# Kernel optimization log

Measured on AMD Instinct MI355X. Metric: run time of the kernel, lower is better.

## Reference

```python
import jax, jax.numpy as jnp
import numpy as np
from jax import lax

DN = ('NCHW', 'OIHW', 'NCHW')

def conv(x, w, b):
    y = lax.conv_general_dilated(x, w, (1, 1), 'VALID', dimension_numbers=DN)
    return y + b[None, :, None, None]

def maxpool2(x):
    return lax.reduce_window(x, -jnp.inf, lax.max, (1, 1, 2, 2), (1, 1, 2, 2), 'VALID')

def setup_inputs() -> dict:
    key = jax.random.key(0)
    ks = jax.random.split(key, 16)
    s = 0.05
    return {
        'x': jax.random.normal(ks[0], (8192, 1, 28, 28), jnp.float32),
        'kf_w1': jax.random.normal(ks[1], (8, 1, 7, 7), jnp.float32) * s,
        'kf_b1': jax.random.normal(ks[2], (8,), jnp.float32) * s,
        'kf_w2': jax.random.normal(ks[3], (10, 8, 5, 5), jnp.float32) * s,
        'kf_b2': jax.random.normal(ks[4], (10,), jnp.float32) * s,
        'kf_fc1_w': jax.random.normal(ks[5], (32, 90), jnp.float32) * s,
        'kf_fc1_b': jax.random.normal(ks[6], (32,), jnp.float32) * s,
        'kf_fc2_w': jax.random.normal(ks[7], (40, 32), jnp.float32) * s,
        'kf_fc2_b': jax.random.normal(ks[8], (40,), jnp.float32) * s,
        'conv2_w': jax.random.normal(ks[9], (20, 10, 5, 5), jnp.float32) * s,
        'conv2_b': jax.random.normal(ks[10], (20,), jnp.float32) * s,
        'fc1_w': jax.random.normal(ks[11], (50, 320), jnp.float32) * s,
        'fc1_b': jax.random.normal(ks[12], (50,), jnp.float32) * s,
        'fc2_w': jax.random.normal(ks[13], (10, 50), jnp.float32) * s,
        'fc2_b': jax.random.normal(ks[14], (10,), jnp.float32) * s,
    }

def _forward(x, kf_w1, kf_b1, kf_w2, kf_b2, kf_fc1_w, kf_fc1_b, kf_fc2_w, kf_fc2_b,
             conv2_w, conv2_b, fc1_w, fc1_b, fc2_w, fc2_b):
    n = x.shape[0]
    # KernelFinder: conv7 -> pool -> relu -> conv5 -> pool -> relu
    f = jax.nn.relu(maxpool2(conv(x, kf_w1, kf_b1)))        # [N,8,11,11]
    f = jax.nn.relu(maxpool2(conv(f, kf_w2, kf_b2)))        # [N,10,3,3]
    f = f.reshape(n, 90)
    h = jax.nn.relu(f @ kf_fc1_w.T + kf_fc1_b)
    kernels = (h @ kf_fc2_w.T + kf_fc2_b).reshape(n, 10, 1, 2, 2)
    # per-sample dynamic conv: each image gets its own [10,1,2,2] kernel
    def one(img, k):
        return lax.conv_general_dilated(img[None], k, (1, 1), 'VALID',
                                        dimension_numbers=DN)[0]
    y = jax.vmap(one)(x, kernels)                           # [N,10,27,27]
    y = jax.nn.relu(maxpool2(y))                            # [N,10,13,13]
    # dropout2d is identity in eval mode
    y = jax.nn.relu(maxpool2(conv(y, conv2_w, conv2_b)))    # [N,20,4,4]
    y = y.reshape(n, 320)
    y = jax.nn.relu(y @ fc1_w.T + fc1_b)
    # F.dropout identity in eval
    y = y @ fc2_w.T + fc2_b
    return jax.nn.log_softmax(y, axis=1)

def reference(x, kf_w1, kf_b1, kf_w2, kf_b2, kf_fc1_w, kf_fc1_b, kf_fc2_w, kf_fc2_b,
              conv2_w, conv2_b, fc1_w, fc1_b, fc2_w, fc2_b):
    return _forward(x, kf_w1, kf_b1, kf_w2, kf_b2, kf_fc1_w, kf_fc1_b, kf_fc2_w,
                    kf_fc2_b, conv2_w, conv2_b, fc1_w, fc1_b, fc2_w, fc2_b)
```

## Files before the change

### kernel.cpp

```cpp
#include <hip/hip_runtime.h>
#include <math.h>

#define TPB 192

typedef __attribute__((ext_vector_type(8))) short bf16x8;
typedef __attribute__((ext_vector_type(4))) float f32x4;

#define OX    0
#define OC1   784
#define OY2   784
#define OF    2656
#define OH    2748
#define OC2S  2656
#define OK2   4960
#define OP3   0
#define OPF   320
#define OA1   420
#define OZ    472
#define SM_TOT 5000

#define W3_ENTRIES 15360

__device__ __forceinline__ unsigned short f2bf(float f) {
    unsigned int u = __float_as_uint(f);
    u += 0x7FFF + ((u >> 16) & 1);
    return (unsigned short)(u >> 16);
}

__global__ void repack_w3(const float* __restrict__ conv2_w,
                          unsigned short* __restrict__ w3)
{
    int i = blockIdx.x * blockDim.x + threadIdx.x;
    if (i >= W3_ENTRIES) return;
    int k  = i & 31;
    int oc = (i >> 5) & 31;
    int g  = i >> 10;
    int kyp = g % 3, kx = g / 3;
    int kyip = k >> 4, ic = k & 15, ky = 2 * kyp + kyip;
    float v = 0.f;
    if (oc < 20 && ic < 10 && ky < 5)
        v = conv2_w[(oc * 10 + ic) * 25 + ky * 5 + kx];
    w3[i] = f2bf(v);
}

__global__ __launch_bounds__(TPB) void fused_forward(
    const float* __restrict__ x,
    const float* __restrict__ kf_w1, const float* __restrict__ kf_b1,
    const float* __restrict__ kf_w2, const float* __restrict__ kf_b2,
    const float* __restrict__ kf_fc1_w, const float* __restrict__ kf_fc1_b,
    const float* __restrict__ kf_fc2_w, const float* __restrict__ kf_fc2_b,
    const float* __restrict__ conv2_w, const float* __restrict__ conv2_b,
    const float* __restrict__ fc1_w, const float* __restrict__ fc1_b,
    const float* __restrict__ fc2_w, const float* __restrict__ fc2_b,
    const unsigned short* __restrict__ w3,
    float* __restrict__ out)
{
    __shared__ __align__(16) float sm[SM_TOT];
    const int tid = threadIdx.x;
    const int n = blockIdx.x;

    {
        const float4* xg = (const float4*)(x + (long long)n * 784);
        float4* d = (float4*)&sm[OX];
        for (int i = tid; i < 196; i += TPB) d[i] = xg[i];
    }
    __syncthreads();

    if (tid < 176) {
        int oc = tid & 7;
        int r  = tid >> 3;
        int py = r >> 1;
        int h  = r & 1;
        const int cc0 = 10 * h;
        float c[2][12];
        #pragma unroll
        for (int r2 = 0; r2 < 2; ++r2)
            #pragma unroll
            for (int i = 0; i < 12; ++i) c[r2][i] = 0.f;
        float wc[7], wp[7];
        const float* wg = kf_w1 + oc * 49;
        #pragma unroll
        for (int i = 0; i < 7; ++i) wc[i] = wg[i];
        #pragma unroll
        for (int t = 0; t < 8; ++t) {
            const float2* xs = (const float2*)&sm[OX + (2 * py + t) * 28 + cc0];
            float row[18];
            #pragma unroll
            for (int i = 0; i < 9; ++i) { float2 q = xs[i]; row[2*i] = q.x; row[2*i+1] = q.y; }
            if (t <= 6) {
                #pragma unroll
                for (int kx = 0; kx < 7; ++kx)
                    #pragma unroll
                    for (int cc = 0; cc < 12; ++cc)
                        c[0][cc] = fmaf(wc[kx], row[cc + kx], c[0][cc]);
            }
            if (t >= 1) {
                #pragma unroll
                for (int kx = 0; kx < 7; ++kx)
                    #pragma unroll
                    for (int cc = 0; cc < 12; ++cc)
                        c[1][cc] = fmaf(wp[kx], row[cc + kx], c[1][cc]);
            }
            #pragma unroll
            for (int i = 0; i < 7; ++i) wp[i] = wc[i];
            if (t < 7) {
                const float* wn = wg + (t + 1) * 7;
                #pragma unroll
                for (int i = 0; i < 7; ++i) wc[i] = wn[i];
            }
        }
        float b = kf_b1[oc];
        #pragma unroll
        for (int j = 0; j < 6; ++j) {
            float m = fmaxf(fmaxf(c[0][2 * j], c[0][2 * j + 1]),
                            fmaxf(c[1][2 * j], c[1][2 * j + 1]));
            sm[OC1 + oc * 132 + py * 12 + 5 * h + j] = fmaxf(m + b, 0.f);
        }
    }
    __syncthreads();

    if (tid < 90) {
        int oc = tid % 10, r = tid / 10;
        int py = r / 3, px = r % 3;
        float a00 = 0.f, a01 = 0.f, a10 = 0.f, a11 = 0.f;
        for (int ic = 0; ic < 8; ++ic) {
            float w[25];
            const float* wg = kf_w2 + (oc * 8 + ic) * 25;
            #pragma unroll
            for (int i = 0; i < 25; ++i) w[i] = wg[i];
            const float* xb = &sm[OC1 + ic * 132 + 2 * py * 12 + 2 * px];
            float cur[6], nxt[6];
            {
                const float2* xr = (const float2*)xb;
                #pragma unroll
                for (int i = 0; i < 3; ++i) { float2 q = xr[i]; cur[2*i] = q.x; cur[2*i+1] = q.y; }
            }
            #pragma unroll
            for (int ky = 0; ky < 5; ++ky) {
                const float2* xr = (const float2*)(xb + (ky + 1) * 12);
                #pragma unroll
                for (int i = 0; i < 3; ++i) { float2 q = xr[i]; nxt[2*i] = q.x; nxt[2*i+1] = q.y; }
                #pragma unroll
                for (int kx = 0; kx < 5; ++kx) {
                    float wv = w[ky * 5 + kx];
                    a00 = fmaf(wv, cur[kx],     a00);
                    a01 = fmaf(wv, cur[kx + 1], a01);
                    a10 = fmaf(wv, nxt[kx],     a10);
                    a11 = fmaf(wv, nxt[kx + 1], a11);
                }
                #pragma unroll
                for (int i = 0; i < 6; ++i) cur[i] = nxt[i];
            }
        }
        float m = fmaxf(fmaxf(a00, a01), fmaxf(a10, a11)) + kf_b2[oc];
        sm[OF + oc * 9 + py * 3 + px] = fmaxf(m, 0.f);
    }
    __syncthreads();

    if (tid < 32) {
        float acc = kf_fc1_b[tid];
        const float2* wr = (const float2*)&kf_fc1_w[tid * 90];
        const float2* ff = (const float2*)&sm[OF];
        for (int i = 0; i < 45; ++i) {
            float2 wv = wr[i], fv = ff[i];
            acc = fmaf(wv.x, fv.x, acc);
            acc = fmaf(wv.y, fv.y, acc);
        }
        sm[OH + tid] = fmaxf(acc, 0.f);
    }
    if (tid < 40) {
        float acc = kf_fc2_b[tid];
        const float4* wr = (const float4*)&kf_fc2_w[tid * 32];
        const float4* hh = (const float4*)&sm[OH];
        #pragma unroll
        for (int i = 0; i < 8; ++i) {
            float4 wv = wr[i], hv = hh[i];
            acc = fmaf(wv.x, hv.x, acc);
            acc = fmaf(wv.y, hv.y, acc);
            acc = fmaf(wv.z, hv.z, acc);
            acc = fmaf(wv.w, hv.w, acc);
        }
        sm[OK2 + tid] = acc;
    }
    if (tid >= 64) {
        float4* z4 = (float4*)&sm[OY2];
        for (int i = tid - 64; i < 468; i += 128) z4[i] = float4{0.f, 0.f, 0.f, 0.f};
    }
    __syncthreads();

    if (tid < 120) {
        int oc = tid % 10, py = tid / 10;
        float4 kv = *(const float4*)&sm[OK2 + oc * 4];
        float k0 = kv.x, k1 = kv.y, k2 = kv.z, k3 = kv.w;
        const float* x0 = &sm[OX + 2 * py * 28];
        const float* x1 = x0 + 28;
        const float* x2 = x0 + 56;
        float2 q0 = *(const float2*)&x0[0];
        float2 q1 = *(const float2*)&x1[0];
        float2 q2 = *(const float2*)&x2[0];
        float A0 = q0.x, B0 = q0.y;
        float A1 = q1.x, B1 = q1.y;
        float A2 = q2.x, B2 = q2.y;
        unsigned short* y2 = (unsigned short*)&sm[OY2];
        #pragma unroll
        for (int j = 0; j < 12; ++j) {
            float2 r0 = *(const float2*)&x0[2 * j + 2];
            float2 r1 = *(const float2*)&x1[2 * j + 2];
            float2 r2v = *(const float2*)&x2[2 * j + 2];
            float C0 = r0.x, C1 = r1.x, C2 = r2v.x;
            float c00 = A0 * k0 + B0 * k1 + A1 * k2 + B1 * k3;
            float c01 = B0 * k0 + C0 * k1 + B1 * k2 + C1 * k3;
            float c10 = A1 * k0 + B1 * k1 + A2 * k2 + B2 * k3;
            float c11 = B1 * k0 + C1 * k1 + B2 * k2 + C2 * k3;
            float m = fmaxf(fmaxf(c00, c01), fmaxf(c10, c11));
            y2[py * 288 + j * 24 + oc] = f2bf(fmaxf(m, 0.f));
            A0 = C0; A1 = C1; A2 = C2;
            B0 = r0.y; B1 = r1.y; B2 = r2v.y;
        }
    }
    __syncthreads();

    {
        const int wv = tid >> 6;
        if (wv < 2) {
            const int l  = tid & 63;
            const int lm = l & 15, lk = l >> 4;
            f32x4 a00 = {0.f, 0.f, 0.f, 0.f};
            f32x4 a01 = a00, a10 = a00, a11 = a00;
            const char* W3 = (const char*)w3;
            const int aoff = (lm * 32 + lk * 8) * 2;
            const int n0 = wv * 32 + lm;
            const int n1 = n0 + 16;
            const int kyip = l >> 5, icb = (lk & 1) * 8;
            const unsigned short* Y2 = (const unsigned short*)&sm[OY2];
            const int b0 = ((n0 >> 3) + kyip) * 288 + (n0 & 7) * 24 + icb;
            const int b1 = ((n1 >> 3) + kyip) * 288 + (n1 & 7) * 24 + icb;
            #pragma unroll
            for (int p = 0; p < 3; ++p) {
                #pragma unroll
                for (int kx = 0; kx < 5; ++kx) {
                    const char* wa = W3 + (kx * 3 + p) * 2048 + aoff;
                    bf16x8 A0 = *(const bf16x8*)wa;
                    bf16x8 A1 = *(const bf16x8*)(wa + 1024);
                    const int bo = p * 576 + kx * 24;
                    bf16x8 B0 = *(const bf16x8*)(Y2 + b0 + bo);
                    bf16x8 B1 = *(const bf16x8*)(Y2 + b1 + bo);
                    a00 = __builtin_amdgcn_mfma_f32_16x16x32_bf16(A0, B0, a00, 0, 0, 0);
                    a01 = __builtin_amdgcn_mfma_f32_16x16x32_bf16(A0, B1, a01, 0, 0, 0);
                    a10 = __builtin_amdgcn_mfma_f32_16x16x32_bf16(A1, B0, a10, 0, 0, 0);
                    a11 = __builtin_amdgcn_mfma_f32_16x16x32_bf16(A1, B1, a11, 0, 0, 0);
                }
            }
            float* C = &sm[OC2S];
            *(f32x4*)(C + n0 * 36 + lk * 4)      = a00;
            *(f32x4*)(C + n1 * 36 + lk * 4)      = a01;
            *(f32x4*)(C + n0 * 36 + 16 + lk * 4) = a10;
            *(f32x4*)(C + n1 * 36 + 16 + lk * 4) = a11;
        }
    }
    __syncthreads();

    if (tid < 80) {
        int oc = tid % 20, py = tid / 20;
        float b = conv2_b[oc];
        const float* C = &sm[OC2S];
        #pragma unroll
        for (int px = 0; px < 4; ++px) {
            int n00 = (2 * py) * 8 + 2 * px;
            float c00 = C[n00 * 36 + oc];
            float c01 = C[(n00 + 1) * 36 + oc];
            float c10 = C[(n00 + 8) * 36 + oc];
            float c11 = C[(n00 + 9) * 36 + oc];
            float m = fmaxf(fmaxf(c00, c01), fmaxf(c10, c11)) + b;
            sm[OP3 + oc * 16 + py * 4 + px] = fmaxf(m, 0.f);
        }
    }
    __syncthreads();

    if (tid < 100) {
        int g = tid / 50, o = tid % 50;
        const float4* wr4 = (const float4*)&fc1_w[o * 320 + g * 160];
        const float4* pp4 = (const float4*)&sm[OP3 + g * 160];
        float acc = 0.f;
        for (int i = 0; i < 40; ++i) {
            float4 wv = wr4[i], pv = pp4[i];
            acc = fmaf(wv.x, pv.x, acc);
            acc = fmaf(wv.y, pv.y, acc);
            acc = fmaf(wv.z, pv.z, acc);
            acc = fmaf(wv.w, pv.w, acc);
        }
        sm[OPF + tid] = acc;
    }
    __syncthreads();

    if (tid < 50) {
        float acc = fc1_b[tid] + sm[OPF + tid] + sm[OPF + 50 + tid];
        sm[OA1 + tid] = fmaxf(acc, 0.f);
    }
    if (tid < 10) {
        float acc = fc2_b[tid];
        const float2* wr = (const float2*)&fc2_w[tid * 50];
        #pragma unroll
        for (int i = 0; i < 25; ++i) {
            float2 wv = wr[i];
            acc = fmaf(wv.x, sm[OA1 + 2 * i], acc);
            acc = fmaf(wv.y, sm[OA1 + 2 * i + 1], acc);
        }
        sm[OZ + tid] = acc;
    }
    if (tid < 10) {
        float m = sm[OZ + 0];
        #pragma unroll
        for (int i = 1; i < 10; ++i) m = fmaxf(m, sm[OZ + i]);
        float s = 0.f;
        #pragma unroll
        for (int i = 0; i < 10; ++i) s += expf(sm[OZ + i] - m);
        out[n * 10 + tid] = sm[OZ + tid] - m - logf(s);
    }
}

extern "C" void kernel_launch(void* const* d_in, const int* in_sizes, int n_in,
                              void* d_out, int out_size, void* d_ws, size_t ws_size,
                              hipStream_t stream) {
    const float* x        = (const float*)d_in[0];
    const float* kf_w1    = (const float*)d_in[1];
    const float* kf_b1    = (const float*)d_in[2];
    const float* kf_w2    = (const float*)d_in[3];
    const float* kf_b2    = (const float*)d_in[4];
    const float* kf_fc1_w = (const float*)d_in[5];
    const float* kf_fc1_b = (const float*)d_in[6];
    const float* kf_fc2_w = (const float*)d_in[7];
    const float* kf_fc2_b = (const float*)d_in[8];
    const float* conv2_w  = (const float*)d_in[9];
    const float* conv2_b  = (const float*)d_in[10];
    const float* fc1_w    = (const float*)d_in[11];
    const float* fc1_b    = (const float*)d_in[12];
    const float* fc2_w    = (const float*)d_in[13];
    const float* fc2_b    = (const float*)d_in[14];

    const int N = in_sizes[0] / 784;

    unsigned short* w3 = (unsigned short*)d_ws;
    repack_w3<<<(W3_ENTRIES + 255) / 256, 256, 0, stream>>>(conv2_w, w3);

    fused_forward<<<N, TPB, 0, stream>>>(
        x, kf_w1, kf_b1, kf_w2, kf_b2, kf_fc1_w, kf_fc1_b, kf_fc2_w, kf_fc2_b,
        conv2_w, conv2_b, fc1_w, fc1_b, fc2_w, fc2_b, w3, (float*)d_out);
}
```

Before: 250.7 us.

## Move KernelFinder conv2 onto bf16 MFMA and compact conv2 weight packing

Conv1 output is now stored in LDS as bf16 in an HWC layout. The second KernelFinder convolution (8->10 channels, 5x5) becomes an implicit GEMM using 16x16x32 bf16 MFMA across three waves, with the 2x2 maxpool and bias applied afterwards. This replaces the per-thread scalar FMA loop that ran on only 90 threads. The conv2_w repack drops the padded output channels 20-31 to shrink the weight buffer, and the second A fragment is clamped. The change adds bf16 rounding to the kernel-finder path, which feeds the dynamic per-sample kernels and may affect accuracy.

New measurement: 230.5 us. 8.0% less time.

```diff
diff --git a/kernel.cpp b/kernel.cpp
--- a/kernel.cpp
+++ b/kernel.cpp
@@ -7,7 +7,8 @@
 typedef __attribute__((ext_vector_type(4))) float f32x4;
 
 #define OX    0
-#define OC1   784
+#define OC1B  784
+#define OC5   1312
 #define OY2   784
 #define OF    2656
 #define OH    2748
@@ -19,7 +20,9 @@
 #define OZ    472
 #define SM_TOT 5000
 
-#define W3_ENTRIES 15360
+#define W3U 0
+#define W5U 9600
+#define WSU_TOT 13184
 
 __device__ __forceinline__ unsigned short f2bf(float f) {
     unsigned int u = __float_as_uint(f);
@@ -27,20 +30,30 @@
     return (unsigned short)(u >> 16);
 }
 
-__global__ void repack_w3(const float* __restrict__ conv2_w,
-                          unsigned short* __restrict__ w3)
+__global__ void repack_w(const float* __restrict__ conv2_w,
+                         const float* __restrict__ kf_w2,
+                         unsigned short* __restrict__ ws)
 {
     int i = blockIdx.x * blockDim.x + threadIdx.x;
-    if (i >= W3_ENTRIES) return;
-    int k  = i & 31;
-    int oc = (i >> 5) & 31;
-    int g  = i >> 10;
-    int kyp = g % 3, kx = g / 3;
-    int kyip = k >> 4, ic = k & 15, ky = 2 * kyp + kyip;
-    float v = 0.f;
-    if (oc < 20 && ic < 10 && ky < 5)
-        v = conv2_w[(oc * 10 + ic) * 25 + ky * 5 + kx];
-    w3[i] = f2bf(v);
+    if (i < 9600) {
+        int g = i / 640, rem = i % 640;
+        int oc = rem >> 5, k = rem & 31;
+        int kyp = g % 3, kx = g / 3;
+        int kyip = k >> 4, ic = k & 15, ky = 2 * kyp + kyip;
+        float v = 0.f;
+        if (ic < 10 && ky < 5)
+            v = conv2_w[(oc * 10 + ic) * 25 + ky * 5 + kx];
+        ws[W3U + i] = f2bf(v);
+    } else if (i < WSU_TOT) {
+        int j = i - 9600;
+        int s = j >> 9, rem = j & 511;
+        int oc = rem >> 5, k = rem & 31;
+        int tap = 4 * s + (k >> 3), ic = k & 7;
+        float v = 0.f;
+        if (oc < 10 && tap < 25)
+            v = kf_w2[(oc * 8 + ic) * 25 + tap];
+        ws[W5U + j] = f2bf(v);
+    }
 }
 
 __global__ __launch_bounds__(TPB) void fused_forward(
@@ -52,7 +65,7 @@
     const float* __restrict__ conv2_w, const float* __restrict__ conv2_b,
     const float* __restrict__ fc1_w, const float* __restrict__ fc1_b,
     const float* __restrict__ fc2_w, const float* __restrict__ fc2_b,
-    const unsigned short* __restrict__ w3,
+    const unsigned short* __restrict__ wsu,
     float* __restrict__ out)
 {
     __shared__ __align__(16) float sm[SM_TOT];
@@ -110,50 +123,46 @@
             }
         }
         float b = kf_b1[oc];
+        unsigned short* c1b = (unsigned short*)&sm[OC1B];
         #pragma unroll
         for (int j = 0; j < 6; ++j) {
             float m = fmaxf(fmaxf(c[0][2 * j], c[0][2 * j + 1]),
                             fmaxf(c[1][2 * j], c[1][2 * j + 1]));
-            sm[OC1 + oc * 132 + py * 12 + 5 * h + j] = fmaxf(m + b, 0.f);
-        }
+            c1b[py * 96 + (5 * h + j) * 8 + oc] = f2bf(fmaxf(m + b, 0.f));
+        }
+    }
+    __syncthreads();
+
+    {
+        const int wv = tid >> 6, l = tid & 63;
+        const int lm = l & 15, lq = l >> 4;
+        int nn = wv * 16 + lm;
+        int nc = nn > 35 ? 35 : nn;
+        const int rr = nc / 6, cc = nc - rr * 6;
+        const unsigned short* c1b = (const unsigned short*)&sm[OC1B];
+        const char* W5 = (const char*)(wsu + W5U);
+        f32x4 acc = {0.f, 0.f, 0.f, 0.f};
+        #pragma unroll
+        for (int s = 0; s < 7; ++s) {
+            int tap = 4 * s + lq;
+            int ky = (tap * 13) >> 6;
+            int kx = tap - ky * 5;
+            bf16x8 A = *(const bf16x8*)(W5 + s * 1024 + lm * 64 + lq * 16);
+            bf16x8 B = *(const bf16x8*)(c1b + (rr + ky) * 96 + (cc + kx) * 8);
+            acc = __builtin_amdgcn_mfma_f32_16x16x32_bf16(A, B, acc, 0, 0, 0);
+        }
+        *(f32x4*)(&sm[OC5] + nn * 20 + lq * 4) = acc;
     }
     __syncthreads();
 
     if (tid < 90) {
-        int oc = tid % 10, r = tid / 10;
-        int py = r / 3, px = r % 3;
-        float a00 = 0.f, a01 = 0.f, a10 = 0.f, a11 = 0.f;
-        for (int ic = 0; ic < 8; ++ic) {
-            float w[25];
-            const float* wg = kf_w2 + (oc * 8 + ic) * 25;
-            #pragma unroll
-            for (int i = 0; i < 25; ++i) w[i] = wg[i];
-            const float* xb = &sm[OC1 + ic * 132 + 2 * py * 12 + 2 * px];
-            float cur[6], nxt[6];
-            {
-                const float2* xr = (const float2*)xb;
-                #pragma unroll
-                for (int i = 0; i < 3; ++i) { float2 q = xr[i]; cur[2*i] = q.x; cur[2*i+1] = q.y; }
-            }
-            #pragma unroll
-            for (int ky = 0; ky < 5; ++ky) {
-                const float2* xr = (const float2*)(xb + (ky + 1) * 12);
-                #pragma unroll
-                for (int i = 0; i < 3; ++i) { float2 q = xr[i]; nxt[2*i] = q.x; nxt[2*i+1] = q.y; }
-                #pragma unroll
-                for (int kx = 0; kx < 5; ++kx) {
-                    float wv = w[ky * 5 + kx];
-                    a00 = fmaf(wv, cur[kx],     a00);
-                    a01 = fmaf(wv, cur[kx + 1], a01);
-                    a10 = fmaf(wv, nxt[kx],     a10);
-                    a11 = fmaf(wv, nxt[kx + 1], a11);
-                }
-                #pragma unroll
-                for (int i = 0; i < 6; ++i) cur[i] = nxt[i];
-            }
-        }
-        float m = fmaxf(fmaxf(a00, a01), fmaxf(a10, a11)) + kf_b2[oc];
-        sm[OF + oc * 9 + py * 3 + px] = fmaxf(m, 0.f);
+        int oc = tid % 10, rr = tid / 10;
+        int py = rr / 3, px = rr % 3;
+        const float* C5 = &sm[OC5];
+        int nb = (2 * py) * 6 + 2 * px;
+        float v = fmaxf(fmaxf(C5[nb * 20 + oc], C5[(nb + 1) * 20 + oc]),
+                        fmaxf(C5[(nb + 6) * 20 + oc], C5[(nb + 7) * 20 + oc]));
+        sm[OF + oc * 9 + rr] = fmaxf(v + kf_b2[oc], 0.f);
     }
     __syncthreads();
 
@@ -227,8 +236,10 @@
             const int lm = l & 15, lk = l >> 4;
             f32x4 a00 = {0.f, 0.f, 0.f, 0.f};
             f32x4 a01 = a00, a10 = a00, a11 = a00;
-            const char* W3 = (const char*)w3;
-            const int aoff = (lm * 32 + lk * 8) * 2;
+            const char* W3 = (const char*)(wsu + W3U);
+            const int aoff0 = lm * 64 + lk * 16;
+            const int oc1 = 16 + (lm < 4 ? lm : 3);
+            const int aoff1 = oc1 * 64 + lk * 16;
             const int n0 = wv * 32 + lm;
             const int n1 = n0 + 16;
             const int kyip = l >> 5, icb = (lk & 1) * 8;
@@ -239,9 +250,9 @@
             for (int p = 0; p < 3; ++p) {
                 #pragma unroll
                 for (int kx = 0; kx < 5; ++kx) {
-                    const char* wa = W3 + (kx * 3 + p) * 2048 + aoff;
-                    bf16x8 A0 = *(const bf16x8*)wa;
-                    bf16x8 A1 = *(const bf16x8*)(wa + 1024);
+                    const char* wa = W3 + (kx * 3 + p) * 1280;
+                    bf16x8 A0 = *(const bf16x8*)(wa + aoff0);
+                    bf16x8 A1 = *(const bf16x8*)(wa + aoff1);
                     const int bo = p * 576 + kx * 24;
                     bf16x8 B0 = *(const bf16x8*)(Y2 + b0 + bo);
                     bf16x8 B1 = *(const bf16x8*)(Y2 + b1 + bo);
@@ -340,10 +351,10 @@
 
     const int N = in_sizes[0] / 784;
 
-    unsigned short* w3 = (unsigned short*)d_ws;
-    repack_w3<<<(W3_ENTRIES + 255) / 256, 256, 0, stream>>>(conv2_w, w3);
+    unsigned short* wsu = (unsigned short*)d_ws;
+    repack_w<<<(WSU_TOT + 255) / 256, 256, 0, stream>>>(conv2_w, kf_w2, wsu);
 
     fused_forward<<<N, TPB, 0, stream>>>(
         x, kf_w1, kf_b1, kf_w2, kf_b2, kf_fc1_w, kf_fc1_b, kf_fc2_w, kf_fc2_b,
-        conv2_w, conv2_b, fc1_w, fc1_b, fc2_w, fc2_b, w3, (float*)d_out);
+        conv2_w, conv2_b, fc1_w, fc1_b, fc2_w, fc2_b, wsu, (float*)d_out);
 }
```
